# Optimization experiments

Hardware: AMD Instinct MI355X
Metric: run time of the kernel (lower is better)

The kernel has to match this reference:

```python
import jax, jax.numpy as jnp
import numpy as np


def setup_inputs() -> dict:
    key = jax.random.key(0)
    k1, k2, k3 = jax.random.split(key, 3)
    S, G, B, C, P = 3, 8, 2048, 512, 64
    node_feats = jax.random.normal(k1, (S, G * B, C), dtype=jnp.float32)
    weight = jax.random.normal(k2, (P, C), dtype=jnp.float32)
    smooth_factor = jax.random.normal(k3, (P,), dtype=jnp.float32)
    return {
        "node_feats": node_feats,
        "weight": weight,
        "smooth_factor": smooth_factor,
        "batch_size": B,
        "num_graphs": G,
    }


def reference(node_feats, weight, smooth_factor, batch_size, num_graphs):
    # node_feats: [S, N_scale, C] (scales stacked; torch version takes a list and cats)
    S, Ns, C = node_feats.shape
    P = weight.shape[0]
    x = node_feats.reshape(-1, C)                       # [N, C], N = S*Ns

    # RBF-style score: (2*c.x - |x|^2 - |c|^2), clamped at 0, scaled by beta
    cx = x @ weight.T                                   # [N, P]
    x_sq = jnp.sum(x * x, axis=1, keepdims=True)        # [N, 1]
    c_sq = jnp.sum(weight * weight, axis=1)[None, :]    # [1, P]
    beta = jax.nn.sigmoid(smooth_factor)                # [P]
    logits = jnp.minimum(2.0 * cx - x_sq - c_sq, 0.0) / beta[None, :]
    assign = jax.nn.softmax(logits, axis=1)             # [N, P]

    # Per-graph weighted sum (uniform batch_list), accumulated across scales:
    # out[g] = sum_{s,n in graph g} assign[s,g,n]^T feats[s,g,n]
    a = assign.reshape(S, num_graphs, batch_size, P)
    f = node_feats.reshape(S, num_graphs, batch_size, C)
    outputs = jnp.einsum('sgnp,sgnc->gpc', a, f)        # [G, P, C]
    return outputs, assign
```

## Files before the change

### kernel.cpp

```cpp
#include <hip/hip_runtime.h>
#include <math.h>

#define S_ 3
#define G_ 8
#define B_ 2048
#define C_ 512
#define P_ 64
#define N_ (S_ * G_ * B_)

typedef __attribute__((ext_vector_type(8))) short short8;
typedef __attribute__((ext_vector_type(4))) float f32x4;
typedef __attribute__((ext_vector_type(4))) unsigned int uint4v;

__device__ __forceinline__ unsigned f2bf1(float f) {
    union { float f; unsigned u; } c; c.f = f;
    unsigned u = c.u;
    u += 0x7fffu + ((u >> 16) & 1u);
    return u >> 16;
}
__device__ __forceinline__ unsigned pk2(float a, float b) {
    return f2bf1(a) | (f2bf1(b) << 16);
}
__device__ __forceinline__ void gl_lds16(const void* g, void* l) {
    __builtin_amdgcn_global_load_lds(
        (const __attribute__((address_space(1))) void*)g,
        (__attribute__((address_space(3))) void*)l, 16, 0, 0);
}

__global__ __launch_bounds__(64) void prep_kernel(
    const float* __restrict__ w, const float* __restrict__ sf,
    unsigned short* __restrict__ wb, float* __restrict__ csq,
    float* __restrict__ rbeta)
{
    const int p = blockIdx.x, l = threadIdx.x;
    const float* wr = w + (size_t)p * C_ + l * 8;
    f32x4 a = *(const f32x4*)wr;
    f32x4 b = *(const f32x4*)(wr + 4);
    float s = a[0]*a[0] + a[1]*a[1] + a[2]*a[2] + a[3]*a[3]
            + b[0]*b[0] + b[1]*b[1] + b[2]*b[2] + b[3]*b[3];
    uint4v pk;
    pk.x = pk2(a[0], a[1]); pk.y = pk2(a[2], a[3]);
    pk.z = pk2(b[0], b[1]); pk.w = pk2(b[2], b[3]);
    *(uint4v*)&wb[(size_t)p * C_ + l * 8] = pk;
#pragma unroll
    for (int off = 1; off < 64; off <<= 1) s += __shfl_xor(s, off, 64);
    if (l == 0) csq[p] = s;
    if (p == 0) rbeta[l] = 1.0f + expf(-sf[l]);
}

__global__ __launch_bounds__(256, 3) void assign_v6(
    const float* __restrict__ x, const unsigned short* __restrict__ wb,
    const float* __restrict__ csq, const float* __restrict__ rbeta,
    float* __restrict__ assign, unsigned short* __restrict__ a_t)
{
    __shared__ __align__(16) float xsb[2][64 * 64];
    __shared__ __align__(16) unsigned short wsb[2][64 * 72];
    __shared__ float xsq_s[64];
    float* lg = &xsb[0][0];

    const int t = threadIdx.x, lane = t & 63, wv = t >> 6;
    const int q = lane >> 4, col = lane & 15;
    const int n0 = blockIdx.x * 64;
    const int ro = lane >> 4, sslot = lane & 15;
    const int wp = t >> 3, wseg = t & 7;

    const float* gx[4];
#pragma unroll
    for (int i = 0; i < 4; ++i) {
        const int row = 16 * wv + 4 * i + ro;
        const int pr  = ((row >> 1) & 7) | (row & 8);
        gx[i] = x + (size_t)(n0 + row) * C_ + ((sslot ^ pr) << 2);
    }
    const int prA = ((col >> 1) & 7) | (col & 8);

    float csqv[4], rbv[4];
#pragma unroll
    for (int nt = 0; nt < 4; ++nt) {
        csqv[nt] = csq[16 * nt + col];
        rbv[nt]  = rbeta[16 * nt + col];
    }

    f32x4 acc[4];
#pragma unroll
    for (int nt = 0; nt < 4; ++nt) acc[nt] = (f32x4){0.f, 0.f, 0.f, 0.f};
    float xsq = 0.f;

    uint4v wr0 = *(const uint4v*)&wb[(size_t)wp * C_ + wseg * 8];
    uint4v wr1 = *(const uint4v*)&wb[(size_t)(wp + 32) * C_ + wseg * 8];
#pragma unroll
    for (int i = 0; i < 4; ++i) gl_lds16(gx[i], &xsb[0][(16 * wv + 4 * i) * 64]);

#pragma unroll
    for (int ch = 0; ch < 8; ++ch) {
        const int cur = ch & 1;
        *(uint4v*)&wsb[cur][wp * 72 + wseg * 8]        = wr0;
        *(uint4v*)&wsb[cur][(wp + 32) * 72 + wseg * 8] = wr1;
        __syncthreads();
        if (ch < 7) {
            const int k0 = (ch + 1) * 64;
            wr0 = *(const uint4v*)&wb[(size_t)wp * C_ + k0 + wseg * 8];
            wr1 = *(const uint4v*)&wb[(size_t)(wp + 32) * C_ + k0 + wseg * 8];
#pragma unroll
            for (int i = 0; i < 4; ++i)
                gl_lds16(gx[i] + k0, &xsb[cur ^ 1][(16 * wv + 4 * i) * 64]);
        }
#pragma unroll
        for (int s = 0; s < 2; ++s) {
            const int g0 = 8 * s + 2 * q;
            f32x4 f0 = *(const f32x4*)&xsb[cur][(16 * wv + col) * 64 + ((g0 ^ prA) << 2)];
            f32x4 f1 = *(const f32x4*)&xsb[cur][(16 * wv + col) * 64 + (((g0 + 1) ^ prA) << 2)];
            xsq += f0.x*f0.x + f0.y*f0.y + f0.z*f0.z + f0.w*f0.w
                 + f1.x*f1.x + f1.y*f1.y + f1.z*f1.z + f1.w*f1.w;
            union { uint4v u; short8 s8; } cv;
            cv.u.x = pk2(f0.x, f0.y); cv.u.y = pk2(f0.z, f0.w);
            cv.u.z = pk2(f1.x, f1.y); cv.u.w = pk2(f1.z, f1.w);
            const int koff = s * 32 + q * 8;
#pragma unroll
            for (int nt = 0; nt < 4; ++nt) {
                short8 bf = *(const short8*)&wsb[cur][(16 * nt + col) * 72 + koff];
                acc[nt] = __builtin_amdgcn_mfma_f32_16x16x32_bf16(cv.s8, bf, acc[nt], 0, 0, 0);
            }
        }
    }

    xsq += __shfl_xor(xsq, 16, 64);
    xsq += __shfl_xor(xsq, 32, 64);
    if (q == 0) xsq_s[16 * wv + col] = xsq;
    __syncthreads();

    float vals[4][4];
#pragma unroll
    for (int reg = 0; reg < 4; ++reg) {
        const int row = 16 * wv + 4 * q + reg;
        const float xq = xsq_s[row];
        float vmax = -3.4e38f;
#pragma unroll
        for (int nt = 0; nt < 4; ++nt) {
            float v = 2.0f * acc[nt][reg] - xq - csqv[nt];
            v = fminf(v, 0.0f) * rbv[nt];
            vals[reg][nt] = v;
            vmax = fmaxf(vmax, v);
        }
#pragma unroll
        for (int off = 1; off < 16; off <<= 1)
            vmax = fmaxf(vmax, __shfl_xor(vmax, off, 64));
        float ss = 0.f;
#pragma unroll
        for (int nt = 0; nt < 4; ++nt) { vals[reg][nt] = __expf(vals[reg][nt] - vmax); ss += vals[reg][nt]; }
#pragma unroll
        for (int off = 1; off < 16; off <<= 1)
            ss += __shfl_xor(ss, off, 64);
        const float inv = 1.0f / ss;
#pragma unroll
        for (int nt = 0; nt < 4; ++nt) vals[reg][nt] *= inv;
    }

#pragma unroll
    for (int reg = 0; reg < 4; ++reg) {
        const int row = 16 * wv + 4 * q + reg;
#pragma unroll
        for (int nt = 0; nt < 4; ++nt) {
            lg[row * 68 + 16 * nt + col] = vals[reg][nt];
            assign[(size_t)(n0 + row) * P_ + 16 * nt + col] = vals[reg][nt];
        }
    }
    __syncthreads();

    const int p = lane;
    float v[16];
#pragma unroll
    for (int i = 0; i < 16; ++i) v[i] = lg[(wv * 16 + i) * 68 + p];
    uint4v d0, d1;
    d0.x = pk2(v[0], v[1]);   d0.y = pk2(v[2], v[3]);
    d0.z = pk2(v[4], v[5]);   d0.w = pk2(v[6], v[7]);
    d1.x = pk2(v[8], v[9]);   d1.y = pk2(v[10], v[11]);
    d1.z = pk2(v[12], v[13]); d1.w = pk2(v[14], v[15]);
    unsigned short* dst = a_t + (size_t)p * N_ + n0 + wv * 16;
    *(uint4v*)dst = d0;
    *(uint4v*)(dst + 8) = d1;
}

__global__ __launch_bounds__(256, 3) void group_v6(
    const float* __restrict__ x, const unsigned short* __restrict__ a_t,
    float* __restrict__ part)
{
    __shared__ __align__(16) float xsb[2][64 * 64];
    __shared__ __align__(16) unsigned short asb[2][64 * 64];

    const int t = threadIdx.x, lane = t & 63, wv = t >> 6;
    const int q = lane >> 4, col = lane & 15;
    const int g = blockIdx.x, ct = blockIdx.y, ks = blockIdx.z;
    const int c0 = ct * 64, sc = ks >> 2, b0 = (ks & 3) * 512;
    const size_t base = (size_t)sc * (G_ * B_) + (size_t)g * B_ + b0;
    const int ro = lane >> 4, sslot = lane & 15;
    const int aro = lane >> 3, aseg = lane & 7;

    const float* gx[4];
#pragma unroll
    for (int i = 0; i < 4; ++i) {
        const int n  = 16 * wv + 4 * i + ro;
        const int pm = ((n >> 3) & 3) | (((n >> 3) & 1) << 2);
        gx[i] = x + (base + n) * C_ + c0 + ((sslot ^ pm) << 2);
    }
    const unsigned short* ga[2];
#pragma unroll
    for (int i = 0; i < 2; ++i) {
        const int p = 16 * wv + 8 * i + aro;
        ga[i] = a_t + (size_t)p * N_ + base + aseg * 8;
    }
    const int cl = 16 * wv + col;
    const int permq = q | ((q & 1) << 2);
    const int cswz  = (((cl >> 2) ^ permq) << 2) | (cl & 3);

    f32x4 acc[4];
#pragma unroll
    for (int mt = 0; mt < 4; ++mt) acc[mt] = (f32x4){0.f, 0.f, 0.f, 0.f};

#pragma unroll
    for (int i = 0; i < 4; ++i) gl_lds16(gx[i], &xsb[0][(16 * wv + 4 * i) * 64]);
#pragma unroll
    for (int i = 0; i < 2; ++i) gl_lds16(ga[i], &asb[0][(16 * wv + 8 * i) * 64]);

#pragma unroll
    for (int ch = 0; ch < 8; ++ch) {
        const int cur = ch & 1;
        __syncthreads();
        if (ch < 7) {
            const int nb = (ch + 1) * 64;
#pragma unroll
            for (int i = 0; i < 4; ++i)
                gl_lds16(gx[i] + (size_t)nb * C_, &xsb[cur ^ 1][(16 * wv + 4 * i) * 64]);
#pragma unroll
            for (int i = 0; i < 2; ++i)
                gl_lds16(ga[i] + nb, &asb[cur ^ 1][(16 * wv + 8 * i) * 64]);
        }
#pragma unroll
        for (int s = 0; s < 2; ++s) {
            const int koff = s * 32 + q * 8;
            float gv[8];
#pragma unroll
            for (int j = 0; j < 8; ++j) gv[j] = xsb[cur][(koff + j) * 64 + cswz];
            union { uint4v u; short8 s8; } cv;
            cv.u.x = pk2(gv[0], gv[1]); cv.u.y = pk2(gv[2], gv[3]);
            cv.u.z = pk2(gv[4], gv[5]); cv.u.w = pk2(gv[6], gv[7]);
#pragma unroll
            for (int mt = 0; mt < 4; ++mt) {
                short8 af = *(const short8*)&asb[cur][(16 * mt + col) * 64 + koff];
                acc[mt] = __builtin_amdgcn_mfma_f32_16x16x32_bf16(af, cv.s8, acc[mt], 0, 0, 0);
            }
        }
    }

    float* pt = part + (((size_t)(g * 8 + ct) * 12) + ks) * 4096;
#pragma unroll
    for (int mt = 0; mt < 4; ++mt)
#pragma unroll
        for (int reg = 0; reg < 4; ++reg) {
            const int p = 16 * mt + 4 * q + reg;
            pt[p * 64 + cl] = acc[mt][reg];
        }
}

__global__ __launch_bounds__(256) void reduce_out(
    const float* __restrict__ part, float* __restrict__ out)
{
    const int idx = blockIdx.x * 256 + threadIdx.x;
    const int g = idx >> 15, r = idx & 32767;
    const int p = r >> 9,  c = r & 511;
    const int ct = c >> 6, cl = c & 63;
    const float* src = part + (((size_t)(g * 8 + ct) * 12)) * 4096 + p * 64 + cl;
    float s = 0.f;
#pragma unroll
    for (int ks = 0; ks < 12; ++ks) s += src[(size_t)ks * 4096];
    out[idx] = s;
}

extern "C" void kernel_launch(void* const* d_in, const int* in_sizes, int n_in,
                              void* d_out, int out_size, void* d_ws, size_t ws_size,
                              hipStream_t stream) {
    const float* x  = (const float*)d_in[0];
    const float* w  = (const float*)d_in[1];
    const float* sf = (const float*)d_in[2];

    float* out    = (float*)d_out;
    float* assign = out + (size_t)G_ * P_ * C_;

    unsigned short* wb    = (unsigned short*)d_ws;
    float*          csq   = (float*)((char*)d_ws + 65536);
    float*          rbeta = (float*)((char*)d_ws + 65792);
    unsigned short* a_t   = (unsigned short*)((char*)d_ws + 66048);
    float*          part  = (float*)((char*)d_ws + 6553600);

    prep_kernel<<<P_, 64, 0, stream>>>(w, sf, wb, csq, rbeta);
    assign_v6<<<N_ / 64, 256, 0, stream>>>(x, wb, csq, rbeta, assign, a_t);
    dim3 gridB(G_, C_ / 64, 12);
    group_v6<<<gridB, 256, 0, stream>>>(x, a_t, part);
    reduce_out<<<(G_ * P_ * C_) / 256, 256, 0, stream>>>(part, out);
}
```

Measured before the change: 185.3 us.

## Stage weights via direct LDS loads, XOR-swizzle LDS tiles, and use explicit vmcnt barriers

Weight tiles in the assign kernel are now copied with global_load_lds instead of passing through registers and a separate LDS store, and both the weight and assignment tiles use an XOR-swizzled 64-wide layout to avoid bank conflicts. The __syncthreads double-buffer handshake is replaced with inline s_waitcnt vmcnt(6)+s_barrier so the next chunk's loads stay in flight while the current chunk is computed. The assign output is written as coalesced float4 rows from LDS. The hand-written waitcnt depends on the exact count of outstanding loads per thread, so a miscount could introduce a race.

```diff
diff --git a/kernel.cpp b/kernel.cpp
--- a/kernel.cpp
+++ b/kernel.cpp
@@ -26,6 +26,9 @@
         (const __attribute__((address_space(1))) void*)g,
         (__attribute__((address_space(3))) void*)l, 16, 0, 0);
 }
+#define WAIT6_BARRIER() asm volatile("s_waitcnt vmcnt(6)\n\ts_barrier" ::: "memory")
+#define WAIT0_BARRIER() asm volatile("s_waitcnt vmcnt(0)\n\ts_barrier" ::: "memory")
+#define RAW_BARRIER()   asm volatile("s_barrier" ::: "memory")
 
 __global__ __launch_bounds__(64) void prep_kernel(
     const float* __restrict__ w, const float* __restrict__ sf,
@@ -48,30 +51,35 @@
     if (p == 0) rbeta[l] = 1.0f + expf(-sf[l]);
 }
 
-__global__ __launch_bounds__(256, 3) void assign_v6(
+__global__ __launch_bounds__(256, 3) void assign_v7(
     const float* __restrict__ x, const unsigned short* __restrict__ wb,
     const float* __restrict__ csq, const float* __restrict__ rbeta,
     float* __restrict__ assign, unsigned short* __restrict__ a_t)
 {
     __shared__ __align__(16) float xsb[2][64 * 64];
-    __shared__ __align__(16) unsigned short wsb[2][64 * 72];
+    __shared__ __align__(16) unsigned short wsb[2][64 * 64];
     __shared__ float xsq_s[64];
     float* lg = &xsb[0][0];
 
     const int t = threadIdx.x, lane = t & 63, wv = t >> 6;
     const int q = lane >> 4, col = lane & 15;
     const int n0 = blockIdx.x * 64;
-    const int ro = lane >> 4, sslot = lane & 15;
-    const int wp = t >> 3, wseg = t & 7;
 
     const float* gx[4];
 #pragma unroll
     for (int i = 0; i < 4; ++i) {
-        const int row = 16 * wv + 4 * i + ro;
+        const int row = 16 * wv + 4 * i + (lane >> 4);
         const int pr  = ((row >> 1) & 7) | (row & 8);
-        gx[i] = x + (size_t)(n0 + row) * C_ + ((sslot ^ pr) << 2);
+        gx[i] = x + (size_t)(n0 + row) * C_ + (((lane & 15) ^ pr) << 2);
+    }
+    const unsigned short* gw[2];
+#pragma unroll
+    for (int i = 0; i < 2; ++i) {
+        const int p = 16 * wv + 8 * i + (lane >> 3);
+        gw[i] = wb + (size_t)p * C_ + (((lane & 7) ^ (p & 7)) * 8);
     }
     const int prA = ((col >> 1) & 7) | (col & 8);
+    const int wg  = col & 7;
 
     float csqv[4], rbv[4];
 #pragma unroll
@@ -85,24 +93,25 @@
     for (int nt = 0; nt < 4; ++nt) acc[nt] = (f32x4){0.f, 0.f, 0.f, 0.f};
     float xsq = 0.f;
 
-    uint4v wr0 = *(const uint4v*)&wb[(size_t)wp * C_ + wseg * 8];
-    uint4v wr1 = *(const uint4v*)&wb[(size_t)(wp + 32) * C_ + wseg * 8];
 #pragma unroll
     for (int i = 0; i < 4; ++i) gl_lds16(gx[i], &xsb[0][(16 * wv + 4 * i) * 64]);
+#pragma unroll
+    for (int i = 0; i < 2; ++i) gl_lds16(gw[i], &wsb[0][(16 * wv + 8 * i) * 64]);
 
 #pragma unroll
     for (int ch = 0; ch < 8; ++ch) {
         const int cur = ch & 1;
-        *(uint4v*)&wsb[cur][wp * 72 + wseg * 8]        = wr0;
-        *(uint4v*)&wsb[cur][(wp + 32) * 72 + wseg * 8] = wr1;
-        __syncthreads();
         if (ch < 7) {
             const int k0 = (ch + 1) * 64;
-            wr0 = *(const uint4v*)&wb[(size_t)wp * C_ + k0 + wseg * 8];
-            wr1 = *(const uint4v*)&wb[(size_t)(wp + 32) * C_ + k0 + wseg * 8];
 #pragma unroll
             for (int i = 0; i < 4; ++i)
                 gl_lds16(gx[i] + k0, &xsb[cur ^ 1][(16 * wv + 4 * i) * 64]);
+#pragma unroll
+            for (int i = 0; i < 2; ++i)
+                gl_lds16(gw[i] + k0, &wsb[cur ^ 1][(16 * wv + 8 * i) * 64]);
+            WAIT6_BARRIER();
+        } else {
+            WAIT0_BARRIER();
         }
 #pragma unroll
         for (int s = 0; s < 2; ++s) {
@@ -114,13 +123,14 @@
             union { uint4v u; short8 s8; } cv;
             cv.u.x = pk2(f0.x, f0.y); cv.u.y = pk2(f0.z, f0.w);
             cv.u.z = pk2(f1.x, f1.y); cv.u.w = pk2(f1.z, f1.w);
-            const int koff = s * 32 + q * 8;
+            const int wgr = 4 * s + q;
 #pragma unroll
             for (int nt = 0; nt < 4; ++nt) {
-                short8 bf = *(const short8*)&wsb[cur][(16 * nt + col) * 72 + koff];
+                short8 bf = *(const short8*)&wsb[cur][(16 * nt + col) * 64 + ((wgr ^ wg) * 8)];
                 acc[nt] = __builtin_amdgcn_mfma_f32_16x16x32_bf16(cv.s8, bf, acc[nt], 0, 0, 0);
             }
         }
+        RAW_BARRIER();
     }
 
     xsq += __shfl_xor(xsq, 16, 64);
@@ -159,12 +169,17 @@
     for (int reg = 0; reg < 4; ++reg) {
         const int row = 16 * wv + 4 * q + reg;
 #pragma unroll
-        for (int nt = 0; nt < 4; ++nt) {
+        for (int nt = 0; nt < 4; ++nt)
             lg[row * 68 + 16 * nt + col] = vals[reg][nt];
-            assign[(size_t)(n0 + row) * P_ + 16 * nt + col] = vals[reg][nt];
-        }
     }
     __syncthreads();
+
+#pragma unroll
+    for (int i = 0; i < 4; ++i) {
+        const int f = i * 256 + t;
+        const int row = f >> 4, sp = (f & 15) * 4;
+        *(f32x4*)(assign + (size_t)(n0 + row) * P_ + sp) = *(const f32x4*)&lg[row * 68 + sp];
+    }
 
     const int p = lane;
     float v[16];
@@ -180,7 +195,7 @@
     *(uint4v*)(dst + 8) = d1;
 }
 
-__global__ __launch_bounds__(256, 3) void group_v6(
+__global__ __launch_bounds__(256, 3) void group_v7(
     const float* __restrict__ x, const unsigned short* __restrict__ a_t,
     float* __restrict__ part)
 {
@@ -192,25 +207,24 @@
     const int g = blockIdx.x, ct = blockIdx.y, ks = blockIdx.z;
     const int c0 = ct * 64, sc = ks >> 2, b0 = (ks & 3) * 512;
     const size_t base = (size_t)sc * (G_ * B_) + (size_t)g * B_ + b0;
-    const int ro = lane >> 4, sslot = lane & 15;
-    const int aro = lane >> 3, aseg = lane & 7;
 
     const float* gx[4];
 #pragma unroll
     for (int i = 0; i < 4; ++i) {
-        const int n  = 16 * wv + 4 * i + ro;
+        const int n  = 16 * wv + 4 * i + (lane >> 4);
         const int pm = ((n >> 3) & 3) | (((n >> 3) & 1) << 2);
-        gx[i] = x + (base + n) * C_ + c0 + ((sslot ^ pm) << 2);
+        gx[i] = x + (base + n) * C_ + c0 + (((lane & 15) ^ pm) << 2);
     }
     const unsigned short* ga[2];
 #pragma unroll
     for (int i = 0; i < 2; ++i) {
-        const int p = 16 * wv + 8 * i + aro;
-        ga[i] = a_t + (size_t)p * N_ + base + aseg * 8;
+        const int p = 16 * wv + 8 * i + (lane >> 3);
+        ga[i] = a_t + (size_t)p * N_ + base + (((lane & 7) ^ (p & 7)) * 8);
     }
     const int cl = 16 * wv + col;
     const int permq = q | ((q & 1) << 2);
     const int cswz  = (((cl >> 2) ^ permq) << 2) | (cl & 3);
+    const int ag    = col & 7;
 
     f32x4 acc[4];
 #pragma unroll
@@ -224,7 +238,6 @@
 #pragma unroll
     for (int ch = 0; ch < 8; ++ch) {
         const int cur = ch & 1;
-        __syncthreads();
         if (ch < 7) {
             const int nb = (ch + 1) * 64;
 #pragma unroll
@@ -233,6 +246,9 @@
 #pragma unroll
             for (int i = 0; i < 2; ++i)
                 gl_lds16(ga[i] + nb, &asb[cur ^ 1][(16 * wv + 8 * i) * 64]);
+            WAIT6_BARRIER();
+        } else {
+            WAIT0_BARRIER();
         }
 #pragma unroll
         for (int s = 0; s < 2; ++s) {
@@ -243,12 +259,14 @@
             union { uint4v u; short8 s8; } cv;
             cv.u.x = pk2(gv[0], gv[1]); cv.u.y = pk2(gv[2], gv[3]);
             cv.u.z = pk2(gv[4], gv[5]); cv.u.w = pk2(gv[6], gv[7]);
+            const int agr = 4 * s + q;
 #pragma unroll
             for (int mt = 0; mt < 4; ++mt) {
-                short8 af = *(const short8*)&asb[cur][(16 * mt + col) * 64 + koff];
+                short8 af = *(const short8*)&asb[cur][(16 * mt + col) * 64 + ((agr ^ ag) * 8)];
                 acc[mt] = __builtin_amdgcn_mfma_f32_16x16x32_bf16(af, cv.s8, acc[mt], 0, 0, 0);
             }
         }
+        RAW_BARRIER();
     }
 
     float* pt = part + (((size_t)(g * 8 + ct) * 12) + ks) * 4096;
@@ -292,8 +310,8 @@
     float*          part  = (float*)((char*)d_ws + 6553600);
 
     prep_kernel<<<P_, 64, 0, stream>>>(w, sf, wb, csq, rbeta);
-    assign_v6<<<N_ / 64, 256, 0, stream>>>(x, wb, csq, rbeta, assign, a_t);
+    assign_v7<<<N_ / 64, 256, 0, stream>>>(x, wb, csq, rbeta, assign, a_t);
     dim3 gridB(G_, C_ / 64, 12);
-    group_v6<<<gridB, 256, 0, stream>>>(x, a_t, part);
+    group_v7<<<gridB, 256, 0, stream>>>(x, a_t, part);
     reduce_out<<<(G_ * P_ * C_) / 256, 256, 0, stream>>>(part, out);
 }
```

Result: no change. 185.9 us (+0.3%).
